# Kernel tuning notes

Hardware: AMD Instinct MI355X
Metric: run time of the kernel (lower is better)

Reference implementation:

```python
import jax, jax.numpy as jnp
import numpy as np

B, H, W = 128, 48, 48
CEN_IN, CEN_OUT, DIR_IN, DIR_OUT, CEN_K, DIR_K = 32, 32, 24, 24, 3, 5
C_IN = CEN_IN + 4 * DIR_IN  # central + 4 directional groups (hor, ver, diag, anti-diag)


def _dwconv(x, k):
    # x: [B, C, H, W], k: [C, kh, kw] depthwise kernels -> SAME-padded depthwise conv
    C = x.shape[1]
    return jax.lax.conv_general_dilated(
        x, k[:, None], window_strides=(1, 1), padding='SAME',
        dimension_numbers=('NCHW', 'OIHW', 'NCHW'), feature_group_count=C)


def setup_inputs() -> dict:
    key = jax.random.key(0)
    ks = jax.random.split(key, 8)
    s = 0.1
    return {
        'x': jax.random.normal(ks[0], (B, C_IN, H, W), dtype=jnp.float32),
        'cen_tensor': jax.random.normal(ks[1], (CEN_IN, CEN_K, CEN_K), dtype=jnp.float32) * s,
        'dir_tensor': jax.random.normal(ks[2], (DIR_IN, DIR_K), dtype=jnp.float32) * s,
        'cen2cen': jax.random.normal(ks[3], (CEN_OUT, CEN_IN), dtype=jnp.float32) * s,
        'par2cen': jax.random.normal(ks[4], (CEN_OUT, DIR_IN), dtype=jnp.float32) * s,
        'dia2cen': jax.random.normal(ks[5], (CEN_OUT, DIR_IN), dtype=jnp.float32) * s,
        'cen2dir': jax.random.normal(ks[6], (DIR_OUT, CEN_IN), dtype=jnp.float32) * s,
        'dir2dir': jax.random.normal(ks[7], (DIR_OUT, DIR_IN), dtype=jnp.float32) * s,
    }


def reference(x, cen_tensor, dir_tensor, cen2cen, par2cen, dia2cen, cen2dir, dir2dir):
    cen_in = cen_tensor.shape[0]
    dir_in, K = dir_tensor.shape
    # split channel groups: [cen | hor | ver | diag | anti-diag]
    xc = x[:, :cen_in]
    xh = x[:, cen_in:cen_in + dir_in]
    xv = x[:, cen_in + dir_in:cen_in + 2 * dir_in]
    xd1 = x[:, cen_in + 2 * dir_in:cen_in + 3 * dir_in]
    xd2 = x[:, cen_in + 3 * dir_in:]
    eye = jnp.eye(K, dtype=x.dtype)
    # --- directional depthwise stage ---
    yc = _dwconv(xc, cen_tensor)                                # full 2D kernel per channel
    yh = _dwconv(xh, dir_tensor[:, None, :])
    yv = _dwconv(xv, dir_tensor[:, :, None])                    # K x 1 vertical line
    yd1 = _dwconv(xd1, dir_tensor[:, :, None] * eye)            # main diagonal line
    yd2 = _dwconv(xd2, dir_tensor[:, :, None] * eye[:, ::-1])   # anti-diagonal line
    # --- directional pointwise (1x1) mixing stage ---
    mix = lambda Wm, t: jnp.einsum('oc,bchw->bohw', Wm, t)
    out_cen = mix(cen2cen, yc) + mix(par2cen, yh + yv) + mix(dia2cen, yd1 + yd2)
    od_cen = mix(cen2dir, yc)
    out_dirs = [od_cen + mix(dir2dir, t) for t in (yh, yv, yd1, yd2)]
    return jnp.concatenate([out_cen] + out_dirs, axis=1)
```

## Files before the change

kernel.cpp:

```cpp
#include <hip/hip_runtime.h>
#include <hip/hip_bf16.h>


namespace {
constexpr int HH = 48, WW = 48, HW = HH * WW;
constexpr int C_IN = 128, C_OUT = 128, NB = 128;
constexpr int RPB = 8;
constexpr int NSTR = HH / RPB;
constexpr int PIX = RPB * WW;
constexpr int NT = 1024;
constexpr int CHK = 8;
constexpr int NCHK = C_IN / CHK;
constexpr int XR = RPB + 4;
constexpr int QR = 17;
constexpr int XQ = CHK * XR * QR;
constexpr int XROWF = QR * 4;
constexpr int YCS = 392;
constexpr size_t M_BYTES = 128 * 128 * 2;
constexpr size_t ZB_OFF = M_BYTES;
}

typedef __attribute__((ext_vector_type(8))) short bf16x8;
typedef __attribute__((ext_vector_type(4))) float f32x4;

__device__ __forceinline__ ushort f2bf(float f) {
    __hip_bfloat16 h = __float2bfloat16(f);
    return *reinterpret_cast<ushort*>(&h);
}

__global__ void build_M(const float* __restrict__ c2c, const float* __restrict__ p2c,
                        const float* __restrict__ d2c, const float* __restrict__ c2d,
                        const float* __restrict__ d2dW, ushort* __restrict__ Mbf) {
    int t = blockIdx.x * 256 + threadIdx.x;
    if (t >= 128 * 128) return;
    int o = t & 127, c = t >> 7;
    float v;
    if (o < 32) {
        if (c < 32)       v = c2c[o * 32 + c];
        else if (c < 56)  v = p2c[o * 24 + c - 32];
        else if (c < 80)  v = p2c[o * 24 + c - 56];
        else if (c < 104) v = d2c[o * 24 + c - 80];
        else              v = d2c[o * 24 + c - 104];
    } else {
        int g = (o - 32) / 24, oo = (o - 32) % 24;
        if (c < 32) v = c2d[oo * 32 + c];
        else {
            int gc = (c - 32) / 24, cc2 = (c - 32) % 24;
            v = (gc == g) ? d2dW[oo * 24 + cc2] : 0.f;
        }
    }
    Mbf[o * 128 + c] = f2bf(v);
}

__global__ __launch_bounds__(NT) void dsc_fused(
    const float* __restrict__ x,
    const float* __restrict__ cen_t,
    const float* __restrict__ dir_t,
    const ushort* __restrict__ Mbf,
    const float* __restrict__ zb,
    float* __restrict__ out)
{
    __shared__ float  xs[2][XQ * 4];
    __shared__ ushort yT[PIX * 128];
    __shared__ ushort ycp[2][CHK * YCS];

    const int tid = threadIdx.x;
    const int b   = blockIdx.x / NSTR;
    const int h0  = (blockIdx.x % NSTR) * RPB;
    const float* __restrict__ xb = x + (size_t)b * C_IN * HW;

    auto stage = [&](int t, int buf) {
        const int c0 = t * CHK;
#pragma unroll
        for (int k = 0; k < 2; ++k) {
            int d = tid + k * NT;
            if (d < XQ) {
                int q  = d % QR;
                int cr = d / QR;
                int r  = cr % XR;
                int c  = cr / XR;
                int gh = h0 - 2 + r;
                bool ok = ((unsigned)gh < (unsigned)HH) && (q < 12);
                const float* src = ok ? (xb + (size_t)(c0 + c) * HW + gh * WW + q * 4) : zb;
                __builtin_amdgcn_global_load_lds(
                    (const __attribute__((address_space(1))) unsigned int*)src,
                    (__attribute__((address_space(3))) unsigned int*)(&xs[buf][0] + (size_t)d * 4),
                    16, 0, 0);
            }
        }
    };

    auto dwconv = [&](int t) {
        const int c0 = t * CHK;
        const int buf = t & 1;
        ushort* yc = ycp[buf];
#pragma unroll
        for (int k = 0; k < 2; ++k) {
            int task = tid + k * NT;
            if (task >= CHK * 192) break;
            int c   = task / 192;
            int pt  = task % 192;
            int row = pt / 24;
            int w0  = pt % 24;
            int cc  = c0 + c;
            const float* xb0 = &xs[buf][(size_t)(c * XR) * XROWF];
            float a0 = 0.f, a1 = 0.f;
            if (cc < 32) {
#pragma unroll
                for (int i = 0; i < 3; ++i) {
                    const float* xr = xb0 + (row + 1 + i) * XROWF;
                    float k0 = cen_t[cc * 9 + i * 3 + 0];
                    float k1 = cen_t[cc * 9 + i * 3 + 1];
                    float k2 = cen_t[cc * 9 + i * 3 + 2];
                    a0 += k0 * xr[(w0 - 1) & 63] + k1 * xr[w0] + k2 * xr[w0 + 1];
                    a1 += k0 * xr[w0 + 23] + k1 * xr[w0 + 24] + k2 * xr[w0 + 25];
                }
            } else if (cc < 56) {
                int cd = cc - 32;
                const float* xr = xb0 + (row + 2) * XROWF;
#pragma unroll
                for (int i = 0; i < 5; ++i) {
                    float tt = dir_t[cd * 5 + i];
                    a0 += tt * xr[(w0 + i - 2) & 63];
                    a1 += tt * xr[w0 + 22 + i];
                }
            } else if (cc < 80) {
                int cd = cc - 56;
#pragma unroll
                for (int i = 0; i < 5; ++i) {
                    float tt = dir_t[cd * 5 + i];
                    const float* xr = xb0 + (row + i) * XROWF;
                    a0 += tt * xr[w0];
                    a1 += tt * xr[w0 + 24];
                }
            } else if (cc < 104) {
                int cd = cc - 80;
#pragma unroll
                for (int i = 0; i < 5; ++i) {
                    float tt = dir_t[cd * 5 + i];
                    const float* xr = xb0 + (row + i) * XROWF;
                    a0 += tt * xr[(w0 + i - 2) & 63];
                    a1 += tt * xr[w0 + 22 + i];
                }
            } else {
                int cd = cc - 104;
#pragma unroll
                for (int i = 0; i < 5; ++i) {
                    float tt = dir_t[cd * 5 + i];
                    const float* xr = xb0 + (row + i) * XROWF;
                    a0 += tt * xr[(w0 + 2 - i) & 63];
                    a1 += tt * xr[w0 + 26 - i];
                }
            }
            int p = row * 48 + w0;
            yc[c * YCS + p]      = f2bf(a0);
            yc[c * YCS + p + 24] = f2bf(a1);
        }
    };

    auto transpose = [&](int t) {
        const ushort* src = ycp[t & 1];
#pragma unroll
        for (int k = 0; k < 2; ++k) {
            int task = tid + k * NT;
            if (task >= 1536) break;
            int cp = task & 3;
            int p  = task >> 2;
            ushort2 s;
            s.x = src[(cp * 2 + 0) * YCS + p];
            s.y = src[(cp * 2 + 1) * YCS + p];
            int gsw = t ^ (p & 7);
            *(ushort2*)((char*)yT + p * 256 + (gsw << 4) + (cp << 2)) = s;
        }
    };

    stage(0, 0);
    __syncthreads();
    for (int t = 0; t < NCHK; ++t) {
        if (t + 1 < NCHK) stage(t + 1, (t + 1) & 1);
        dwconv(t);
        if (t > 0) transpose(t - 1);
        __syncthreads();
    }
    transpose(NCHK - 1);
    __syncthreads();

    const int l   = tid & 63;
    const int wv  = tid >> 6;
    const int ofr = wv & 3;
    const int pq  = wv >> 2;
    float* __restrict__ ob = out + (size_t)b * C_OUT * HW + h0 * WW;

#pragma unroll
    for (int pass = 0; pass < 2; ++pass) {
        int o0 = pass * 64 + ofr * 16;
        bf16x8 afr[4];
#pragma unroll
        for (int kb = 0; kb < 4; ++kb)
            afr[kb] = *(const bf16x8*)(Mbf + (o0 + (l & 15)) * 128 + kb * 32 + (l >> 4) * 8);
        f32x4 acc[6] = {};
#pragma unroll
        for (int kb = 0; kb < 4; ++kb) {
            int g = kb * 4 + (l >> 4);
#pragma unroll
            for (int pf = 0; pf < 6; ++pf) {
                int p = (pq * 6 + pf) * 16 + (l & 15);
                const bf16x8 bfr = *(const bf16x8*)((const char*)yT + p * 256 + ((g ^ (p & 7)) << 4));
                acc[pf] = __builtin_amdgcn_mfma_f32_16x16x32_bf16(afr[kb], bfr, acc[pf], 0, 0, 0);
            }
        }
#pragma unroll
        for (int pf = 0; pf < 6; ++pf) {
            int p = (pq * 6 + pf) * 16 + (l & 15);
            int obase = o0 + (l >> 4) * 4;
#pragma unroll
            for (int r = 0; r < 4; ++r)
                ob[(size_t)(obase + r) * HW + p] = acc[pf][r];
        }
    }
}

extern "C" void kernel_launch(void* const* d_in, const int* in_sizes, int n_in,
                              void* d_out, int out_size, void* d_ws, size_t ws_size,
                              hipStream_t stream) {
    const float* x     = (const float*)d_in[0];
    const float* cen_t = (const float*)d_in[1];
    const float* dir_t = (const float*)d_in[2];
    const float* c2c   = (const float*)d_in[3];
    const float* p2c   = (const float*)d_in[4];
    const float* d2c   = (const float*)d_in[5];
    const float* c2d   = (const float*)d_in[6];
    const float* d2dW  = (const float*)d_in[7];
    float* out = (float*)d_out;

    ushort* Mbf = (ushort*)d_ws;
    float*  zb  = (float*)((char*)d_ws + ZB_OFF);

    hipMemsetAsync(zb, 0, 64, stream);
    build_M<<<64, 256, 0, stream>>>(c2c, p2c, d2c, c2d, d2dW, Mbf);
    dsc_fused<<<NB * NSTR, NT, 0, stream>>>(x, cen_t, dir_t, Mbf, zb, out);
}
```

Baseline: 115.7 us.

## Halve block threads and hand-schedule async LDS staging with explicit waits

Cuts the block from 1024 to 512 threads, so each thread handles three staging, dwconv and transpose tasks and twice as many MFMA accumulator tiles. The staging row pitch changes from 17 to 16 quads so index math becomes shifts and bounds checks disappear. __syncthreads is replaced with explicit vmcnt/lgkmcnt waits, raw s_barrier and sched_barrier fences, so the next chunk's global-to-LDS load can stay in flight during the current dwconv. The aim is lower barrier and address overhead with better load overlap, at the cost of more registers per thread, possible LDS bank conflicts from the power-of-two pitch, and relying on hand-counted vmcnt values for correctness.

```diff
diff --git a/kernel.cpp b/kernel.cpp
--- a/kernel.cpp
+++ b/kernel.cpp
@@ -8,11 +8,11 @@
 constexpr int RPB = 8;
 constexpr int NSTR = HH / RPB;
 constexpr int PIX = RPB * WW;
-constexpr int NT = 1024;
+constexpr int NT = 512;
 constexpr int CHK = 8;
 constexpr int NCHK = C_IN / CHK;
 constexpr int XR = RPB + 4;
-constexpr int QR = 17;
+constexpr int QR = 16;
 constexpr int XQ = CHK * XR * QR;
 constexpr int XROWF = QR * 4;
 constexpr int YCS = 392;
@@ -27,6 +27,11 @@
     __hip_bfloat16 h = __float2bfloat16(f);
     return *reinterpret_cast<ushort*>(&h);
 }
+
+#define SCHED_FENCE() __builtin_amdgcn_sched_barrier(0)
+#define WAIT_VM(N) do { asm volatile("s_waitcnt vmcnt(" #N ")" ::: "memory"); SCHED_FENCE(); } while (0)
+#define BAR() do { __builtin_amdgcn_s_barrier(); SCHED_FENCE(); } while (0)
+#define WAIT_LGKM() do { asm volatile("s_waitcnt lgkmcnt(0)" ::: "memory"); SCHED_FENCE(); } while (0)
 
 __global__ void build_M(const float* __restrict__ c2c, const float* __restrict__ p2c,
                         const float* __restrict__ d2c, const float* __restrict__ c2d,
@@ -72,21 +77,19 @@
     auto stage = [&](int t, int buf) {
         const int c0 = t * CHK;
 #pragma unroll
-        for (int k = 0; k < 2; ++k) {
+        for (int k = 0; k < 3; ++k) {
             int d = tid + k * NT;
-            if (d < XQ) {
-                int q  = d % QR;
-                int cr = d / QR;
-                int r  = cr % XR;
-                int c  = cr / XR;
-                int gh = h0 - 2 + r;
-                bool ok = ((unsigned)gh < (unsigned)HH) && (q < 12);
-                const float* src = ok ? (xb + (size_t)(c0 + c) * HW + gh * WW + q * 4) : zb;
-                __builtin_amdgcn_global_load_lds(
-                    (const __attribute__((address_space(1))) unsigned int*)src,
-                    (__attribute__((address_space(3))) unsigned int*)(&xs[buf][0] + (size_t)d * 4),
-                    16, 0, 0);
-            }
+            int q  = d & 15;
+            int cr = d >> 4;
+            int r  = cr % XR;
+            int c  = cr / XR;
+            int gh = h0 - 2 + r;
+            bool ok = ((unsigned)gh < (unsigned)HH) && (q < 12);
+            const float* src = ok ? (xb + (size_t)(c0 + c) * HW + gh * WW + q * 4) : zb;
+            __builtin_amdgcn_global_load_lds(
+                (const __attribute__((address_space(1))) unsigned int*)src,
+                (__attribute__((address_space(3))) unsigned int*)(&xs[buf][0] + (size_t)d * 4),
+                16, 0, 0);
         }
     };
 
@@ -95,9 +98,8 @@
         const int buf = t & 1;
         ushort* yc = ycp[buf];
 #pragma unroll
-        for (int k = 0; k < 2; ++k) {
+        for (int k = 0; k < 3; ++k) {
             int task = tid + k * NT;
-            if (task >= CHK * 192) break;
             int c   = task / 192;
             int pt  = task % 192;
             int row = pt / 24;
@@ -161,9 +163,8 @@
     auto transpose = [&](int t) {
         const ushort* src = ycp[t & 1];
 #pragma unroll
-        for (int k = 0; k < 2; ++k) {
+        for (int k = 0; k < 3; ++k) {
             int task = tid + k * NT;
-            if (task >= 1536) break;
             int cp = task & 3;
             int p  = task >> 2;
             ushort2 s;
@@ -175,20 +176,30 @@
     };
 
     stage(0, 0);
-    __syncthreads();
-    for (int t = 0; t < NCHK; ++t) {
-        if (t + 1 < NCHK) stage(t + 1, (t + 1) & 1);
+    SCHED_FENCE();
+    for (int t = 0; t < NCHK - 1; ++t) {
+        stage(t + 1, (t + 1) & 1);
+        SCHED_FENCE();
+        WAIT_VM(3);
+        BAR();
         dwconv(t);
         if (t > 0) transpose(t - 1);
-        __syncthreads();
+        WAIT_LGKM();
+        BAR();
     }
+    WAIT_VM(0);
+    BAR();
+    dwconv(NCHK - 1);
+    transpose(NCHK - 2);
+    WAIT_LGKM();
+    BAR();
     transpose(NCHK - 1);
     __syncthreads();
 
-    const int l   = tid & 63;
-    const int wv  = tid >> 6;
-    const int ofr = wv & 3;
-    const int pq  = wv >> 2;
+    const int l     = tid & 63;
+    const int wv    = tid >> 6;
+    const int ofr   = wv & 3;
+    const int phalf = wv >> 2;
     float* __restrict__ ob = out + (size_t)b * C_OUT * HW + h0 * WW;
 
 #pragma unroll
@@ -198,20 +209,20 @@
 #pragma unroll
         for (int kb = 0; kb < 4; ++kb)
             afr[kb] = *(const bf16x8*)(Mbf + (o0 + (l & 15)) * 128 + kb * 32 + (l >> 4) * 8);
-        f32x4 acc[6] = {};
+        f32x4 acc[12] = {};
 #pragma unroll
         for (int kb = 0; kb < 4; ++kb) {
             int g = kb * 4 + (l >> 4);
 #pragma unroll
-            for (int pf = 0; pf < 6; ++pf) {
-                int p = (pq * 6 + pf) * 16 + (l & 15);
+            for (int pf = 0; pf < 12; ++pf) {
+                int p = (phalf * 12 + pf) * 16 + (l & 15);
                 const bf16x8 bfr = *(const bf16x8*)((const char*)yT + p * 256 + ((g ^ (p & 7)) << 4));
                 acc[pf] = __builtin_amdgcn_mfma_f32_16x16x32_bf16(afr[kb], bfr, acc[pf], 0, 0, 0);
             }
         }
 #pragma unroll
-        for (int pf = 0; pf < 6; ++pf) {
-            int p = (pq * 6 + pf) * 16 + (l & 15);
+        for (int pf = 0; pf < 12; ++pf) {
+            int p = (phalf * 12 + pf) * 16 + (l & 15);
             int obase = o0 + (l >> 4) * 4;
 #pragma unroll
             for (int r = 0; r < 4; ++r)
```

Result: slower. 122.2 us (+5.6%).
